# Kernel optimization log

Hardware: AMD Instinct MI355X
Metric: run time of the kernel (lower is better)

The kernel has to match this reference:

```python
import jax, jax.numpy as jnp
import numpy as np

D_MODEL = 1024

def setup_inputs() -> dict:
    key = jax.random.key(0)
    kx, kq, kk, kv, ko = jax.random.split(key, 5)
    x = jax.random.normal(kx, (4, 4096, D_MODEL), dtype=jnp.float32)
    w_q = jax.random.normal(kq, (D_MODEL, D_MODEL), dtype=jnp.float32)
    w_k = jax.random.normal(kk, (D_MODEL, D_MODEL), dtype=jnp.float32)
    w_v = jax.random.normal(kv, (D_MODEL, D_MODEL), dtype=jnp.float32)
    w_o = jax.random.normal(ko, (D_MODEL, D_MODEL), dtype=jnp.float32)
    return {"x": x, "w_q": w_q, "w_k": w_k, "w_v": w_v, "w_o": w_o}

def reference(x, w_q, w_k, w_v, w_o):
    # Q/K/V projections: [B,T,D] @ [D,D] -> [B,T,D]
    q = jnp.einsum('btd,de->bte', x, w_q)
    k = jnp.einsum('btd,de->bte', x, w_k)
    v = jnp.einsum('btd,de->bte', x, w_v)
    # Unnormalized attention: scores [B,T,T] (no softmax)
    scores = jnp.einsum('btd,bsd->bts', q, k)
    attn_output = jnp.einsum('bts,bsd->btd', scores, v)
    # Output projection
    output = jnp.einsum('btd,de->bte', attn_output, w_o)
    return output
```

## Files before the change

### kernel.cpp

```cpp
#include <hip/hip_runtime.h>
#include <hip/hip_bf16.h>
#include <stdint.h>

typedef unsigned short u16;
typedef short bf16x8 __attribute__((ext_vector_type(8)));
typedef float f32x4 __attribute__((ext_vector_type(4)));

#define GLOAD16(gp, lp) __builtin_amdgcn_global_load_lds( \
    (const __attribute__((address_space(1))) uint32_t*)(gp), \
    (__attribute__((address_space(3))) uint32_t*)(lp), 16, 0, 0)

#define VMCNT10 do { asm volatile("s_waitcnt vmcnt(10)" ::: "memory"); \
                     __builtin_amdgcn_sched_barrier(0); } while (0)
#define SBAR    do { __builtin_amdgcn_s_barrier(); \
                     __builtin_amdgcn_sched_barrier(0); } while (0)
#define LGKM0   do { asm volatile("s_waitcnt lgkmcnt(0)" ::: "memory"); \
                     __builtin_amdgcn_sched_barrier(0); } while (0)

__device__ __forceinline__ u16 f2bf(float f) {
  union { float f; uint32_t u; } x; x.f = f;
  return (u16)((x.u + 0x7FFFu + ((x.u >> 16) & 1u)) >> 16);
}
__device__ __forceinline__ float bf2f(u16 h) {
  union { uint32_t u; float f; } x; x.u = (uint32_t)h << 16;
  return x.f;
}

__device__ __forceinline__ void xcd_swizzle(int& bx, int& by, int& bz) {
  const int gx = gridDim.x, gy = gridDim.y;
  const int nwg = gx * gy * (int)gridDim.z;
  const int lin = ((int)blockIdx.z * gy + (int)blockIdx.y) * gx + (int)blockIdx.x;
  const int q = nwg >> 3;
  const int wl = (lin & 7) * q + (lin >> 3);
  bz = wl / (gx * gy);
  const int rem = wl - bz * gx * gy;
  by = rem / gx;
  bx = rem - by * gx;
}

__global__ __launch_bounds__(256) void cast_x_tr(const float* __restrict__ x,
                                                 u16* __restrict__ xb,
                                                 u16* __restrict__ xT) {
  __shared__ float tile[64][65];
  const int t = threadIdx.x;
  const int lr = t >> 2, lc = (t & 3) * 16;
  const int d0 = blockIdx.x * 64;
  const int t0 = blockIdx.y * 64;
  const float* src = x + (size_t)(t0 + lr) * 1024 + d0 + lc;
  u16 pl[16];
#pragma unroll
  for (int j = 0; j < 4; ++j) {
    float4 v = *(const float4*)&src[j * 4];
    tile[lr][lc + j * 4 + 0] = v.x;
    tile[lr][lc + j * 4 + 1] = v.y;
    tile[lr][lc + j * 4 + 2] = v.z;
    tile[lr][lc + j * 4 + 3] = v.w;
    pl[j * 4 + 0] = f2bf(v.x); pl[j * 4 + 1] = f2bf(v.y);
    pl[j * 4 + 2] = f2bf(v.z); pl[j * 4 + 3] = f2bf(v.w);
  }
  u16* pdst = xb + (size_t)(t0 + lr) * 1024 + d0 + lc;
  *(uint4*)&pdst[0] = *(const uint4*)&pl[0];
  *(uint4*)&pdst[8] = *(const uint4*)&pl[8];
  __syncthreads();
  u16 tr[16];
#pragma unroll
  for (int j = 0; j < 16; ++j) tr[j] = f2bf(tile[lc + j][lr]);
  u16* tdst = xT + (size_t)(d0 + lr) * 16384 + t0 + lc;
  *(uint4*)&tdst[0] = *(const uint4*)&tr[0];
  *(uint4*)&tdst[8] = *(const uint4*)&tr[8];
}

__global__ __launch_bounds__(256) void cast_weights(const float* __restrict__ wq,
                                                    const float* __restrict__ wk,
                                                    const float* __restrict__ wv,
                                                    const float* __restrict__ wo,
                                                    u16* __restrict__ WA,
                                                    u16* __restrict__ WBb) {
  __shared__ float tile[64][65];
  const int z = blockIdx.z;
  const float* in = z == 0 ? wq : z == 1 ? wk : z == 2 ? wv : wo;
  u16* o = z == 0 ? WA : z == 1 ? WBb : z == 2 ? WBb + 1048576 : WA + 1048576;
  const int t = threadIdx.x;
  const int lr = t >> 2, lc = (t & 3) * 16;
  const int r0 = blockIdx.y * 64, c0 = blockIdx.x * 64;
  const float* src = in + (size_t)(r0 + lr) * 1024 + c0 + lc;
  if (z < 3) {
    u16 p[16];
#pragma unroll
    for (int j = 0; j < 4; ++j) {
      float4 v = *(const float4*)&src[j * 4];
      p[j * 4 + 0] = f2bf(v.x); p[j * 4 + 1] = f2bf(v.y);
      p[j * 4 + 2] = f2bf(v.z); p[j * 4 + 3] = f2bf(v.w);
    }
    u16* dst = o + (size_t)(r0 + lr) * 1024 + c0 + lc;
    *(uint4*)&dst[0] = *(const uint4*)&p[0];
    *(uint4*)&dst[8] = *(const uint4*)&p[8];
  } else {
#pragma unroll
    for (int j = 0; j < 4; ++j) {
      float4 v = *(const float4*)&src[j * 4];
      tile[lr][lc + j * 4 + 0] = v.x;
      tile[lr][lc + j * 4 + 1] = v.y;
      tile[lr][lc + j * 4 + 2] = v.z;
      tile[lr][lc + j * 4 + 3] = v.w;
    }
    __syncthreads();
    u16 tr[16];
#pragma unroll
    for (int j = 0; j < 16; ++j) tr[j] = f2bf(tile[lc + j][lr]);
    u16* dst = o + (size_t)(c0 + lr) * 1024 + r0 + lc;
    *(uint4*)&dst[0] = *(const uint4*)&tr[0];
    *(uint4*)&dst[8] = *(const uint4*)&tr[8];
  }
}

__global__ __launch_bounds__(512) void gemm_bt8(const u16* __restrict__ A,
                                                const u16* __restrict__ B,
                                                u16* __restrict__ C,
                                                int lda, int ldb, int ldc, int K,
                                                size_t sA, size_t sB, size_t sC) {
  __shared__ u16 lds[2 * 8192];
  int bx, by, bz;
  xcd_swizzle(bx, by, bz);
  A += (size_t)bz * sA;
  B += (size_t)bz * sB;
  const int t = threadIdx.x;
  const int l = t & 63;
  const int wid = t >> 6;
  const int wr = wid >> 2, wc = wid & 3;
  const int lr16 = l & 15, hi = l >> 4;
  const int mBase = by * 128;
  const int nBase = bx * 128;

  f32x4 acc[4][2];
#pragma unroll
  for (int m = 0; m < 4; ++m)
#pragma unroll
    for (int n = 0; n < 2; ++n) acc[m][n] = (f32x4){0.f, 0.f, 0.f, 0.f};

  for (int kt = 0; kt < K; kt += 64) {
    __syncthreads();
#pragma unroll
    for (int i = 0; i < 2; ++i) {
      int s = i * 512 + t;
      int row = s >> 3, cp = s & 7;
      int clog = cp ^ (row & 7);
      GLOAD16(A + (size_t)(mBase + row) * lda + kt + clog * 8, &lds[s * 8]);
    }
#pragma unroll
    for (int i = 0; i < 2; ++i) {
      int s = i * 512 + t;
      int row = s >> 3, cp = s & 7;
      int clog = cp ^ (row & 7);
      GLOAD16(B + (size_t)(nBase + row) * ldb + kt + clog * 8, &lds[8192 + s * 8]);
    }
    asm volatile("s_waitcnt vmcnt(0)" ::: "memory");
    __syncthreads();
#pragma unroll
    for (int ks = 0; ks < 2; ++ks) {
      bf16x8 af[4], bfr[2];
#pragma unroll
      for (int m = 0; m < 4; ++m) {
        int row = wr * 64 + m * 16 + lr16;
        int p = (ks * 4 + hi) ^ (row & 7);
        af[m] = *(const bf16x8*)&lds[row * 64 + p * 8];
      }
#pragma unroll
      for (int n = 0; n < 2; ++n) {
        int row = wc * 32 + n * 16 + lr16;
        int p = (ks * 4 + hi) ^ (row & 7);
        bfr[n] = *(const bf16x8*)&lds[8192 + row * 64 + p * 8];
      }
#pragma unroll
      for (int m = 0; m < 4; ++m)
#pragma unroll
        for (int n = 0; n < 2; ++n)
          acc[m][n] = __builtin_amdgcn_mfma_f32_16x16x32_bf16(af[m], bfr[n], acc[m][n], 0, 0, 0);
    }
  }

#pragma unroll
  for (int m = 0; m < 4; ++m) {
    int row0 = mBase + wr * 64 + m * 16 + hi * 4;
#pragma unroll
    for (int n = 0; n < 2; ++n) {
      int col = nBase + wc * 32 + n * 16 + lr16;
      f32x4 v = acc[m][n];
      u16* Cb = C + (size_t)bz * sC;
#pragma unroll
      for (int r = 0; r < 4; ++r) Cb[(size_t)(row0 + r) * ldc + col] = f2bf(v[r]);
    }
  }
}

template <bool F32OUT>
__device__ __forceinline__ void gemm256_core(const u16* __restrict__ A,
                                             const u16* __restrict__ B,
                                             void* __restrict__ C,
                                             int lda, int ldb, int ldc, int K,
                                             int mBase, int nBase, u16* lds) {
  const int t = threadIdx.x;
  const int l = t & 63;
  const int wid = t >> 6;
  const int wr = wid >> 2;
  const int wc = wid & 3;
  const int lr16 = l & 15, hi = l >> 4;
  const int rl0 = t >> 3;
  const int rl1 = rl0 + 64;
  const int cp  = t & 7;
  const int cs  = cp ^ (rl0 & 7);
  const int NT = K >> 6;

  f32x4 acc[8][4];
#pragma unroll
  for (int m = 0; m < 8; ++m)
#pragma unroll
    for (int n = 0; n < 4; ++n) acc[m][n] = (f32x4){0.f, 0.f, 0.f, 0.f};

  auto stage = [&](const u16* g0, int ld, u16* d) {
    GLOAD16(g0 + (size_t)rl0 * ld + cs * 8, d + rl0 * 64 + cp * 8);
    GLOAD16(g0 + (size_t)rl1 * ld + cs * 8, d + rl1 * 64 + cp * 8);
  };
  stage(A + (size_t)mBase * lda,          lda, lds + 0);
  stage(B + (size_t)nBase * ldb,          ldb, lds + 16384);
  stage(B + (size_t)(nBase + 128) * ldb,  ldb, lds + 24576);
  stage(A + (size_t)(mBase + 128) * lda,  lda, lds + 8192);
  stage(B + (size_t)nBase * ldb + 64,         ldb, lds + 32768 + 16384);
  stage(A + (size_t)mBase * lda + 64,         lda, lds + 32768);
  stage(B + (size_t)(nBase + 128) * ldb + 64, ldb, lds + 32768 + 24576);

  bf16x8 af[4][2], b0[2][2], b1[2][2];

  for (int tt = 0; tt < NT; ++tt) {
    const int cur = tt & 1;
    u16* bufA = lds + cur * 32768;
    u16* bufB = bufA + 16384;
    u16* bufN = lds + ((tt + 1) & 1) * 32768;
    int t1 = tt + 1; if (t1 >= NT) t1 -= NT;
    int t2 = tt + 2; if (t2 >= NT) t2 -= NT;
    const int k1 = t1 * 64, k2 = t2 * 64;

    VMCNT10;
    SBAR;
    stage(A + (size_t)(mBase + 128) * lda + k1, lda, bufN + 8192);
#pragma unroll
    for (int mi = 0; mi < 4; ++mi) {
      int row = wr * 64 + mi * 16 + lr16;
#pragma unroll
      for (int kk = 0; kk < 2; ++kk) {
        int p = (kk * 4 + hi) ^ (row & 7);
        af[mi][kk] = *(const bf16x8*)&bufA[row * 64 + p * 8];
      }
    }
#pragma unroll
    for (int ni = 0; ni < 2; ++ni) {
      int row = wc * 32 + ni * 16 + lr16;
#pragma unroll
      for (int kk = 0; kk < 2; ++kk) {
        int p = (kk * 4 + hi) ^ (row & 7);
        b0[ni][kk] = *(const bf16x8*)&bufB[row * 64 + p * 8];
      }
    }
    LGKM0;
    __builtin_amdgcn_s_setprio(1);
#pragma unroll
    for (int kk = 0; kk < 2; ++kk)
#pragma unroll
      for (int mi = 0; mi < 4; ++mi)
#pragma unroll
        for (int ni = 0; ni < 2; ++ni)
          acc[mi][ni] = __builtin_amdgcn_mfma_f32_16x16x32_bf16(af[mi][kk], b0[ni][kk], acc[mi][ni], 0, 0, 0);
    __builtin_amdgcn_s_setprio(0);

    VMCNT10;
    SBAR;
    stage(B + (size_t)nBase * ldb + k2, ldb, bufB);
#pragma unroll
    for (int ni = 0; ni < 2; ++ni) {
      int row = 128 + wc * 32 + ni * 16 + lr16;
#pragma unroll
      for (int kk = 0; kk < 2; ++kk) {
        int p = (kk * 4 + hi) ^ (row & 7);
        b1[ni][kk] = *(const bf16x8*)&bufB[row * 64 + p * 8];
      }
    }
    LGKM0;
    __builtin_amdgcn_s_setprio(1);
#pragma unroll
    for (int kk = 0; kk < 2; ++kk)
#pragma unroll
      for (int mi = 0; mi < 4; ++mi)
#pragma unroll
        for (int ni = 0; ni < 2; ++ni)
          acc[mi][2 + ni] = __builtin_amdgcn_mfma_f32_16x16x32_bf16(af[mi][kk], b1[ni][kk], acc[mi][2 + ni], 0, 0, 0);
    __builtin_amdgcn_s_setprio(0);

    VMCNT10;
    SBAR;
    stage(A + (size_t)mBase * lda + k2, lda, bufA);
#pragma unroll
    for (int mi = 0; mi < 4; ++mi) {
      int row = 128 + wr * 64 + mi * 16 + lr16;
#pragma unroll
      for (int kk = 0; kk < 2; ++kk) {
        int p = (kk * 4 + hi) ^ (row & 7);
        af[mi][kk] = *(const bf16x8*)&bufA[row * 64 + p * 8];
      }
    }
    LGKM0;
    __builtin_amdgcn_s_setprio(1);
#pragma unroll
    for (int kk = 0; kk < 2; ++kk)
#pragma unroll
      for (int mi = 0; mi < 4; ++mi)
#pragma unroll
        for (int ni = 0; ni < 2; ++ni)
          acc[4 + mi][2 + ni] = __builtin_amdgcn_mfma_f32_16x16x32_bf16(af[mi][kk], b1[ni][kk], acc[4 + mi][2 + ni], 0, 0, 0);
    __builtin_amdgcn_s_setprio(0);

    SBAR;
    stage(B + (size_t)(nBase + 128) * ldb + k2, ldb, bufB + 8192);
    __builtin_amdgcn_s_setprio(1);
#pragma unroll
    for (int kk = 0; kk < 2; ++kk)
#pragma unroll
      for (int mi = 0; mi < 4; ++mi)
#pragma unroll
        for (int ni = 0; ni < 2; ++ni)
          acc[4 + mi][ni] = __builtin_amdgcn_mfma_f32_16x16x32_bf16(af[mi][kk], b0[ni][kk], acc[4 + mi][ni], 0, 0, 0);
    __builtin_amdgcn_s_setprio(0);
  }

#pragma unroll
  for (int m = 0; m < 8; ++m) {
    int row0 = mBase + (m >> 2) * 128 + wr * 64 + (m & 3) * 16 + hi * 4;
#pragma unroll
    for (int n = 0; n < 4; ++n) {
      int col = nBase + (n >> 1) * 128 + wc * 32 + (n & 1) * 16 + lr16;
      f32x4 v = acc[m][n];
      if (F32OUT) {
        float* Cf = (float*)C;
#pragma unroll
        for (int r = 0; r < 4; ++r) Cf[(size_t)(row0 + r) * ldc + col] = v[r];
      } else {
        u16* Cb = (u16*)C;
#pragma unroll
        for (int r = 0; r < 4; ++r) Cb[(size_t)(row0 + r) * ldc + col] = f2bf(v[r]);
      }
    }
  }
}

__global__ __launch_bounds__(512) void gemm256_out(const u16* __restrict__ xb,
                                                   const u16* __restrict__ PT,
                                                   float* __restrict__ out) {
  __shared__ u16 lds[65536];
  int bx, by, bz;
  xcd_swizzle(bx, by, bz);
  const u16* Bp = PT + (size_t)(by >> 4) * 1048576;
  gemm256_core<true>(xb, Bp, out, 1024, 1024, 1024, 1024, by * 256, bx * 256, lds);
}

__global__ __launch_bounds__(512) void gemm256_gram(const u16* __restrict__ xT,
                                                    u16* __restrict__ Gp) {
  __shared__ u16 lds[65536];
  int bx, by, bz;
  xcd_swizzle(bx, by, bz);
  const int b = bz >> 2, kc = bz & 3;
  const u16* Ap = xT + (size_t)b * 4096 + (size_t)kc * 1024;
  gemm256_core<false>(Ap, Ap, Gp + (size_t)bz * 1048576, 16384, 16384, 1024, 1024,
                      by * 256, bx * 256, lds);
}

__global__ void reduce_gram(const u16* __restrict__ Gp, u16* __restrict__ G) {
  const size_t MW = 1048576;
  int b = blockIdx.y;
  size_t i = ((size_t)blockIdx.x * 256 + threadIdx.x) * 8;
  const u16* p = Gp + (size_t)b * 4 * MW + i;
  u16 a0[8], a1[8], a2[8], a3[8], o[8];
  *(uint4*)a0 = *(const uint4*)&p[0];
  *(uint4*)a1 = *(const uint4*)&p[MW];
  *(uint4*)a2 = *(const uint4*)&p[2 * MW];
  *(uint4*)a3 = *(const uint4*)&p[3 * MW];
#pragma unroll
  for (int j = 0; j < 8; ++j)
    o[j] = f2bf(bf2f(a0[j]) + bf2f(a1[j]) + bf2f(a2[j]) + bf2f(a3[j]));
  *(uint4*)&G[b * MW + i] = *(const uint4*)o;
}

extern "C" void kernel_launch(void* const* d_in, const int* in_sizes, int n_in,
                              void* d_out, int out_size, void* d_ws, size_t ws_size,
                              hipStream_t stream) {
  const float* x  = (const float*)d_in[0];
  const float* wq = (const float*)d_in[1];
  const float* wk = (const float*)d_in[2];
  const float* wv = (const float*)d_in[3];
  const float* wo = (const float*)d_in[4];
  float* out = (float*)d_out;

  u16* ws = (u16*)d_ws;
  const size_t MW = 1048576;
  u16* xb  = ws;
  u16* xT  = ws + 16 * MW;
  u16* WA  = ws + 32 * MW;
  u16* WBb = ws + 34 * MW;
  u16* W12 = ws + 36 * MW;
  u16* G   = ws + 38 * MW;
  u16* S   = ws + 42 * MW;
  u16* PT  = ws + 46 * MW;
  u16* Gp  = ws + 50 * MW;

  cast_x_tr<<<dim3(16, 256), 256, 0, stream>>>(x, xb, xT);
  cast_weights<<<dim3(16, 16, 4), 256, 0, stream>>>(wq, wk, wv, wo, WA, WBb);

  gemm_bt8<<<dim3(8, 8, 2), 512, 0, stream>>>(WA, WBb, W12,
                                              1024, 1024, 1024, 1024,
                                              MW, MW, MW);
  gemm256_gram<<<dim3(4, 4, 16), 512, 0, stream>>>(xT, Gp);
  reduce_gram<<<dim3(512, 4), 256, 0, stream>>>(Gp, G);

  gemm_bt8<<<dim3(8, 8, 4), 512, 0, stream>>>(W12 + MW, G, S,
                                              1024, 1024, 1024, 1024,
                                              0, MW, MW);
  gemm_bt8<<<dim3(8, 8, 4), 512, 0, stream>>>(S, W12, PT,
                                              1024, 1024, 1024, 1024,
                                              MW, 0, MW);
  gemm256_out<<<dim3(4, 64), 512, 0, stream>>>(xb, PT, out);
}
```

Before: 170.8 us.

## Compute only lower-triangle Gram tiles and mirror during reduction; fuse cast kernels

Result: faster. 164.5 us (-3.7%).

```diff
diff --git a/kernel.cpp b/kernel.cpp
--- a/kernel.cpp
+++ b/kernel.cpp
@@ -38,64 +38,24 @@
   bx = rem - by * gx;
 }
 
-__global__ __launch_bounds__(256) void cast_x_tr(const float* __restrict__ x,
-                                                 u16* __restrict__ xb,
-                                                 u16* __restrict__ xT) {
+__global__ __launch_bounds__(256) void cast_all(const float* __restrict__ x,
+                                                const float* __restrict__ wq,
+                                                const float* __restrict__ wk,
+                                                const float* __restrict__ wv,
+                                                const float* __restrict__ wo,
+                                                u16* __restrict__ xb,
+                                                u16* __restrict__ xT,
+                                                u16* __restrict__ WA,
+                                                u16* __restrict__ WBb) {
   __shared__ float tile[64][65];
+  const int lin = blockIdx.x;
   const int t = threadIdx.x;
   const int lr = t >> 2, lc = (t & 3) * 16;
-  const int d0 = blockIdx.x * 64;
-  const int t0 = blockIdx.y * 64;
-  const float* src = x + (size_t)(t0 + lr) * 1024 + d0 + lc;
-  u16 pl[16];
-#pragma unroll
-  for (int j = 0; j < 4; ++j) {
-    float4 v = *(const float4*)&src[j * 4];
-    tile[lr][lc + j * 4 + 0] = v.x;
-    tile[lr][lc + j * 4 + 1] = v.y;
-    tile[lr][lc + j * 4 + 2] = v.z;
-    tile[lr][lc + j * 4 + 3] = v.w;
-    pl[j * 4 + 0] = f2bf(v.x); pl[j * 4 + 1] = f2bf(v.y);
-    pl[j * 4 + 2] = f2bf(v.z); pl[j * 4 + 3] = f2bf(v.w);
-  }
-  u16* pdst = xb + (size_t)(t0 + lr) * 1024 + d0 + lc;
-  *(uint4*)&pdst[0] = *(const uint4*)&pl[0];
-  *(uint4*)&pdst[8] = *(const uint4*)&pl[8];
-  __syncthreads();
-  u16 tr[16];
-#pragma unroll
-  for (int j = 0; j < 16; ++j) tr[j] = f2bf(tile[lc + j][lr]);
-  u16* tdst = xT + (size_t)(d0 + lr) * 16384 + t0 + lc;
-  *(uint4*)&tdst[0] = *(const uint4*)&tr[0];
-  *(uint4*)&tdst[8] = *(const uint4*)&tr[8];
-}
-
-__global__ __launch_bounds__(256) void cast_weights(const float* __restrict__ wq,
-                                                    const float* __restrict__ wk,
-                                                    const float* __restrict__ wv,
-                                                    const float* __restrict__ wo,
-                                                    u16* __restrict__ WA,
-                                                    u16* __restrict__ WBb) {
-  __shared__ float tile[64][65];
-  const int z = blockIdx.z;
-  const float* in = z == 0 ? wq : z == 1 ? wk : z == 2 ? wv : wo;
-  u16* o = z == 0 ? WA : z == 1 ? WBb : z == 2 ? WBb + 1048576 : WA + 1048576;
-  const int t = threadIdx.x;
-  const int lr = t >> 2, lc = (t & 3) * 16;
-  const int r0 = blockIdx.y * 64, c0 = blockIdx.x * 64;
-  const float* src = in + (size_t)(r0 + lr) * 1024 + c0 + lc;
-  if (z < 3) {
-    u16 p[16];
-#pragma unroll
-    for (int j = 0; j < 4; ++j) {
-      float4 v = *(const float4*)&src[j * 4];
-      p[j * 4 + 0] = f2bf(v.x); p[j * 4 + 1] = f2bf(v.y);
-      p[j * 4 + 2] = f2bf(v.z); p[j * 4 + 3] = f2bf(v.w);
-    }
-    u16* dst = o + (size_t)(r0 + lr) * 1024 + c0 + lc;
-    *(uint4*)&dst[0] = *(const uint4*)&p[0];
-    *(uint4*)&dst[8] = *(const uint4*)&p[8];
-  } else {
+  if (lin < 4096) {
+    const int d0 = (lin & 15) * 64;
+    const int t0 = (lin >> 4) * 64;
+    const float* src = x + (size_t)(t0 + lr) * 1024 + d0 + lc;
+    u16 pl[16];
 #pragma unroll
     for (int j = 0; j < 4; ++j) {
       float4 v = *(const float4*)&src[j * 4];
@@ -103,14 +63,54 @@
       tile[lr][lc + j * 4 + 1] = v.y;
       tile[lr][lc + j * 4 + 2] = v.z;
       tile[lr][lc + j * 4 + 3] = v.w;
-    }
+      pl[j * 4 + 0] = f2bf(v.x); pl[j * 4 + 1] = f2bf(v.y);
+      pl[j * 4 + 2] = f2bf(v.z); pl[j * 4 + 3] = f2bf(v.w);
+    }
+    u16* pdst = xb + (size_t)(t0 + lr) * 1024 + d0 + lc;
+    *(uint4*)&pdst[0] = *(const uint4*)&pl[0];
+    *(uint4*)&pdst[8] = *(const uint4*)&pl[8];
     __syncthreads();
     u16 tr[16];
 #pragma unroll
     for (int j = 0; j < 16; ++j) tr[j] = f2bf(tile[lc + j][lr]);
-    u16* dst = o + (size_t)(c0 + lr) * 1024 + r0 + lc;
-    *(uint4*)&dst[0] = *(const uint4*)&tr[0];
-    *(uint4*)&dst[8] = *(const uint4*)&tr[8];
+    u16* tdst = xT + (size_t)(d0 + lr) * 16384 + t0 + lc;
+    *(uint4*)&tdst[0] = *(const uint4*)&tr[0];
+    *(uint4*)&tdst[8] = *(const uint4*)&tr[8];
+  } else {
+    const int w = lin - 4096;
+    const int z = w >> 8, tl = w & 255;
+    const int r0 = (tl >> 4) * 64, c0 = (tl & 15) * 64;
+    const float* in = z == 0 ? wq : z == 1 ? wk : z == 2 ? wv : wo;
+    u16* o = z == 0 ? WA : z == 1 ? WBb : z == 2 ? WBb + 1048576 : WA + 1048576;
+    const float* src = in + (size_t)(r0 + lr) * 1024 + c0 + lc;
+    if (z < 3) {
+      u16 p[16];
+#pragma unroll
+      for (int j = 0; j < 4; ++j) {
+        float4 v = *(const float4*)&src[j * 4];
+        p[j * 4 + 0] = f2bf(v.x); p[j * 4 + 1] = f2bf(v.y);
+        p[j * 4 + 2] = f2bf(v.z); p[j * 4 + 3] = f2bf(v.w);
+      }
+      u16* dst = o + (size_t)(r0 + lr) * 1024 + c0 + lc;
+      *(uint4*)&dst[0] = *(const uint4*)&p[0];
+      *(uint4*)&dst[8] = *(const uint4*)&p[8];
+    } else {
+#pragma unroll
+      for (int j = 0; j < 4; ++j) {
+        float4 v = *(const float4*)&src[j * 4];
+        tile[lr][lc + j * 4 + 0] = v.x;
+        tile[lr][lc + j * 4 + 1] = v.y;
+        tile[lr][lc + j * 4 + 2] = v.z;
+        tile[lr][lc + j * 4 + 3] = v.w;
+      }
+      __syncthreads();
+      u16 tr[16];
+#pragma unroll
+      for (int j = 0; j < 16; ++j) tr[j] = f2bf(tile[lc + j][lr]);
+      u16* dst = o + (size_t)(c0 + lr) * 1024 + r0 + lc;
+      *(uint4*)&dst[0] = *(const uint4*)&tr[0];
+      *(uint4*)&dst[8] = *(const uint4*)&tr[8];
+    }
   }
 }
 
@@ -193,6 +193,128 @@
   }
 }
 
+__global__ __launch_bounds__(512) void gram_tri(const u16* __restrict__ xT,
+                                                u16* __restrict__ Gp) {
+  __shared__ u16 lds[2 * 8192];
+  const int lin = blockIdx.x;
+  const int wl = (lin & 7) * 72 + (lin >> 3);
+  const int z = wl / 36, t5 = wl - z * 36;
+  const int b = z >> 2, kc = z & 3;
+  int ti = 0;
+  while ((ti + 1) * (ti + 2) / 2 <= t5) ++ti;
+  const int tj = t5 - ti * (ti + 1) / 2;
+  const u16* Ap = xT + (size_t)b * 4096 + (size_t)kc * 1024;
+  const int lda = 16384;
+  const int mBase = ti * 128, nBase = tj * 128;
+
+  const int t = threadIdx.x;
+  const int l = t & 63;
+  const int wid = t >> 6;
+  const int wr = wid >> 2, wc = wid & 3;
+  const int lr16 = l & 15, hi = l >> 4;
+
+  f32x4 acc[4][2];
+#pragma unroll
+  for (int m = 0; m < 4; ++m)
+#pragma unroll
+    for (int n = 0; n < 2; ++n) acc[m][n] = (f32x4){0.f, 0.f, 0.f, 0.f};
+
+  for (int kt = 0; kt < 1024; kt += 64) {
+    __syncthreads();
+#pragma unroll
+    for (int i = 0; i < 2; ++i) {
+      int s = i * 512 + t;
+      int row = s >> 3, cp = s & 7;
+      int clog = cp ^ (row & 7);
+      GLOAD16(Ap + (size_t)(mBase + row) * lda + kt + clog * 8, &lds[s * 8]);
+    }
+#pragma unroll
+    for (int i = 0; i < 2; ++i) {
+      int s = i * 512 + t;
+      int row = s >> 3, cp = s & 7;
+      int clog = cp ^ (row & 7);
+      GLOAD16(Ap + (size_t)(nBase + row) * lda + kt + clog * 8, &lds[8192 + s * 8]);
+    }
+    asm volatile("s_waitcnt vmcnt(0)" ::: "memory");
+    __syncthreads();
+#pragma unroll
+    for (int ks = 0; ks < 2; ++ks) {
+      bf16x8 af[4], bfr[2];
+#pragma unroll
+      for (int m = 0; m < 4; ++m) {
+        int row = wr * 64 + m * 16 + lr16;
+        int p = (ks * 4 + hi) ^ (row & 7);
+        af[m] = *(const bf16x8*)&lds[row * 64 + p * 8];
+      }
+#pragma unroll
+      for (int n = 0; n < 2; ++n) {
+        int row = wc * 32 + n * 16 + lr16;
+        int p = (ks * 4 + hi) ^ (row & 7);
+        bfr[n] = *(const bf16x8*)&lds[8192 + row * 64 + p * 8];
+      }
+#pragma unroll
+      for (int m = 0; m < 4; ++m)
+#pragma unroll
+        for (int n = 0; n < 2; ++n)
+          acc[m][n] = __builtin_amdgcn_mfma_f32_16x16x32_bf16(af[m], bfr[n], acc[m][n], 0, 0, 0);
+    }
+  }
+
+  u16* Cb = Gp + ((size_t)z * 36 + t5) * 16384;
+#pragma unroll
+  for (int m = 0; m < 4; ++m) {
+    int row0 = wr * 64 + m * 16 + hi * 4;
+#pragma unroll
+    for (int n = 0; n < 2; ++n) {
+      int col = wc * 32 + n * 16 + lr16;
+      f32x4 v = acc[m][n];
+#pragma unroll
+      for (int r = 0; r < 4; ++r) Cb[(size_t)(row0 + r) * 128 + col] = f2bf(v[r]);
+    }
+  }
+}
+
+__global__ __launch_bounds__(256) void reduce_mirror(const u16* __restrict__ Gp,
+                                                     u16* __restrict__ G) {
+  __shared__ u16 ldsT[128][136];
+  const int t5 = blockIdx.x;
+  const int b = blockIdx.y;
+  int ti = 0;
+  while ((ti + 1) * (ti + 2) / 2 <= t5) ++ti;
+  const int tj = t5 - ti * (ti + 1) / 2;
+  const int tid = threadIdx.x;
+  const int rr = tid >> 4, ccc = (tid & 15) * 8;
+  u16* Gb = G + (size_t)b * 1048576;
+  const size_t ZS = (size_t)36 * 16384;
+  const u16* base = Gp + ((size_t)(b * 4) * 36 + t5) * 16384;
+#pragma unroll
+  for (int i = 0; i < 8; ++i) {
+    int row = i * 16 + rr;
+    const u16* p = base + row * 128 + ccc;
+    u16 a0[8], a1[8], a2[8], a3[8], o[8];
+    *(uint4*)a0 = *(const uint4*)&p[0];
+    *(uint4*)a1 = *(const uint4*)&p[ZS];
+    *(uint4*)a2 = *(const uint4*)&p[2 * ZS];
+    *(uint4*)a3 = *(const uint4*)&p[3 * ZS];
+#pragma unroll
+    for (int j = 0; j < 8; ++j)
+      o[j] = f2bf(bf2f(a0[j]) + bf2f(a1[j]) + bf2f(a2[j]) + bf2f(a3[j]));
+    *(uint4*)&Gb[(size_t)(ti * 128 + row) * 1024 + tj * 128 + ccc] = *(const uint4*)o;
+    *(uint4*)&ldsT[row][ccc] = *(const uint4*)o;
+  }
+  if (ti != tj) {
+    __syncthreads();
+#pragma unroll
+    for (int i = 0; i < 8; ++i) {
+      int row = i * 16 + rr;
+      u16 m8[8];
+#pragma unroll
+      for (int j = 0; j < 8; ++j) m8[j] = ldsT[ccc + j][row];
+      *(uint4*)&Gb[(size_t)(tj * 128 + row) * 1024 + ti * 128 + ccc] = *(const uint4*)m8;
+    }
+  }
+}
+
 template <bool F32OUT>
 __device__ __forceinline__ void gemm256_core(const u16* __restrict__ A,
                                              const u16* __restrict__ B,
@@ -361,33 +483,6 @@
   gemm256_core<true>(xb, Bp, out, 1024, 1024, 1024, 1024, by * 256, bx * 256, lds);
 }
 
-__global__ __launch_bounds__(512) void gemm256_gram(const u16* __restrict__ xT,
-                                                    u16* __restrict__ Gp) {
-  __shared__ u16 lds[65536];
-  int bx, by, bz;
-  xcd_swizzle(bx, by, bz);
-  const int b = bz >> 2, kc = bz & 3;
-  const u16* Ap = xT + (size_t)b * 4096 + (size_t)kc * 1024;
-  gemm256_core<false>(Ap, Ap, Gp + (size_t)bz * 1048576, 16384, 16384, 1024, 1024,
-                      by * 256, bx * 256, lds);
-}
-
-__global__ void reduce_gram(const u16* __restrict__ Gp, u16* __restrict__ G) {
-  const size_t MW = 1048576;
-  int b = blockIdx.y;
-  size_t i = ((size_t)blockIdx.x * 256 + threadIdx.x) * 8;
-  const u16* p = Gp + (size_t)b * 4 * MW + i;
-  u16 a0[8], a1[8], a2[8], a3[8], o[8];
-  *(uint4*)a0 = *(const uint4*)&p[0];
-  *(uint4*)a1 = *(const uint4*)&p[MW];
-  *(uint4*)a2 = *(const uint4*)&p[2 * MW];
-  *(uint4*)a3 = *(const uint4*)&p[3 * MW];
-#pragma unroll
-  for (int j = 0; j < 8; ++j)
-    o[j] = f2bf(bf2f(a0[j]) + bf2f(a1[j]) + bf2f(a2[j]) + bf2f(a3[j]));
-  *(uint4*)&G[b * MW + i] = *(const uint4*)o;
-}
-
 extern "C" void kernel_launch(void* const* d_in, const int* in_sizes, int n_in,
                               void* d_out, int out_size, void* d_ws, size_t ws_size,
                               hipStream_t stream) {
@@ -410,14 +505,13 @@
   u16* PT  = ws + 46 * MW;
   u16* Gp  = ws + 50 * MW;
 
-  cast_x_tr<<<dim3(16, 256), 256, 0, stream>>>(x, xb, xT);
-  cast_weights<<<dim3(16, 16, 4), 256, 0, stream>>>(wq, wk, wv, wo, WA, WBb);
+  cast_all<<<5120, 256, 0, stream>>>(x, wq, wk, wv, wo, xb, xT, WA, WBb);
 
   gemm_bt8<<<dim3(8, 8, 2), 512, 0, stream>>>(WA, WBb, W12,
                                               1024, 1024, 1024, 1024,
                                               MW, MW, MW);
-  gemm256_gram<<<dim3(4, 4, 16), 512, 0, stream>>>(xT, Gp);
-  reduce_gram<<<dim3(512, 4), 256, 0, stream>>>(Gp, G);
+  gram_tri<<<576, 512, 0, stream>>>(xT, Gp);
+  reduce_mirror<<<dim3(36, 4), 256, 0, stream>>>(Gp, G);
 
   gemm_bt8<<<dim3(8, 8, 4), 512, 0, stream>>>(W12 + MW, G, S,
                                               1024, 1024, 1024, 1024,
```
